# Kernel tuning notes

Measured on AMD Instinct MI355X. Metric: run time of the kernel, lower is better.

Reference implementation:

```python
import jax, jax.numpy as jnp
import numpy as np

J0 = -0.1
J1 = 0.1
ALPHA = 0.15
BUMP_WIDTH_FACTOR = 10.0


def _w_delta7(n):
    idx = jnp.arange(n, dtype=jnp.float32)
    angle_diff = 2.0 * jnp.pi * (idx[:, None] - idx[None, :]) / n
    return jnp.cos(angle_diff)  # [N, N]


def _initial_bump(batch_size, n):
    # initial angle = pi for every batch element (matches r_init=None path)
    angles = jnp.full((batch_size,), jnp.pi, dtype=jnp.float32)
    centers = (angles * n / (2.0 * jnp.pi))[:, None]          # [B, 1]
    width = n / BUMP_WIDTH_FACTOR
    idx = jnp.arange(n, dtype=jnp.float32)[None, :]            # [1, N]
    d = jnp.abs(idx - centers)
    dist = jnp.minimum(d, n - d)                               # circular distance
    bump = jnp.exp(-(dist ** 2) / (2.0 * width ** 2))
    return bump / jnp.linalg.norm(bump, axis=1, keepdims=True)  # [B, N]


def setup_inputs() -> dict:
    key = jax.random.key(0)
    k1, k2, k3 = jax.random.split(key, 3)
    B, S, A, N = 64, 256, 32, 256
    action_signal = jax.random.normal(k1, (B, S, A), dtype=jnp.float32)
    Wo = jax.random.normal(k2, (N, N), dtype=jnp.float32) / np.sqrt(N)
    Wa = jax.random.normal(k3, (A, N, N), dtype=jnp.float32) / np.sqrt(N)
    return {"action_signal": action_signal, "Wo": Wo, "Wa": Wa}


def reference(action_signal, Wo, Wa):
    B, S, A = action_signal.shape
    N = Wo.shape[0]
    W_delta7 = _w_delta7(N)
    r0 = _initial_bump(B, N)
    # static part of the effective weight matrix: J1*W_delta7 + Wo
    W_static = J1 * W_delta7 + Wo  # [N, N]

    def step(r, a_t):
        # a_t: [B, A], r: [B, N]
        # W_eff = J0 + W_static + sum_a a_t[a]*Wa[a]; rec = W_eff @ r (per batch)
        Wa_weighted = jnp.einsum('ba,anm->bnm', a_t, Wa)       # [B, N, N]
        rec = (J0 * jnp.sum(r, axis=-1, keepdims=True)
               + r @ W_static.T
               + jnp.einsum('bnm,bm->bn', Wa_weighted, r))      # [B, N]
        r_new = (1.0 - ALPHA) * r + ALPHA * jax.nn.relu(rec)
        return r_new, r_new

    _, bumps = jax.lax.scan(step, r0, jnp.swapaxes(action_signal, 0, 1))
    bump_history = jnp.swapaxes(bumps, 0, 1)                   # [B, S, N]
    r_delta7 = bump_history @ W_delta7                          # [B, S, N]
    r_history = r_delta7 / jnp.max(r_delta7, axis=2, keepdims=True)
    return r_history, bump_history
```

## Files before the change

kernel.cpp:

```cpp
#include <hip/hip_runtime.h>
#include <math.h>

#define N_    256
#define B_    64
#define S_    256
#define A_    32
#define NSZ   8
#define BSZ   8
#define LROWS 18
#define ATS   12
#define AROWS 33
#define J0_   (-0.1f)
#define J1_   (0.1f)
#define ALPHA_ 0.15f
#define WIDTH_ 25.6f
#define TWO_PI 6.283185307179586f

#define RPAR      (BSZ * N_)
#define RGRP      (2 * RPAR)
#define FLAG_OFF  (8 * RGRP)

#define WA_LDS_FLOATS (NSZ * LROWS * N_)
#define AT_LDS_FLOATS (2 * AROWS * ATS)
#define RLDS_FLOATS   (RPAR)
#define LDS_BYTES ((WA_LDS_FLOATS + AT_LDS_FLOATS + RLDS_FLOATS) * 4)

#define NN ((size_t)N_ * N_)

typedef float v2f __attribute__((ext_vector_type(2)));

#define LOADX4_COH(dst, p) \
  asm volatile("global_load_dwordx4 %0, %1, off sc0 sc1" \
               : "=v"(dst) : "v"(p) : "memory")
#define LOADX4(dst, p) \
  asm volatile("global_load_dwordx4 %0, %1, off" : "=v"(dst) : "v"(p) : "memory")
#define WAIT_VM0() asm volatile("s_waitcnt vmcnt(0)" ::: "memory")

#define ROWFMA(wvec, a_idx) do {                                              \
    const float* atp_ = atb + (a_idx) * ATS;                                  \
    const float4 t0_ = *reinterpret_cast<const float4*>(atp_);                \
    const float4 t1_ = *reinterpret_cast<const float4*>(atp_ + 4);            \
    const v2f at0_ = {t0_.x, t0_.y}, at1_ = {t0_.z, t0_.w};                   \
    const v2f at2_ = {t1_.x, t1_.y}, at3_ = {t1_.z, t1_.w};                   \
    const v2f wx_ = {(wvec).x, (wvec).x}, wy_ = {(wvec).y, (wvec).y};         \
    const v2f wz_ = {(wvec).z, (wvec).z}, ww_ = {(wvec).w, (wvec).w};         \
    const v2f d0_ = wx_*rrp[0][0] + wy_*rrp[0][1] + wz_*rrp[0][2] + ww_*rrp[0][3]; \
    const v2f d1_ = wx_*rrp[1][0] + wy_*rrp[1][1] + wz_*rrp[1][2] + ww_*rrp[1][3]; \
    const v2f d2_ = wx_*rrp[2][0] + wy_*rrp[2][1] + wz_*rrp[2][2] + ww_*rrp[2][3]; \
    const v2f d3_ = wx_*rrp[3][0] + wy_*rrp[3][1] + wz_*rrp[3][2] + ww_*rrp[3][3]; \
    accp[0] += at0_ * d0_;  accp[1] += at1_ * d1_;                            \
    accp[2] += at2_ * d2_;  accp[3] += at3_ * d3_;                            \
  } while (0)

__device__ __forceinline__ float bumpval(float idx) {
  float d = fabsf(idx - 128.0f);
  d = fminf(d, 256.0f - d);
  return expf(-d * d / (2.0f * WIDTH_ * WIDTH_));
}

__global__ __launch_bounds__(512, 1)
void ring_scan_kernel(const float* __restrict__ action,
                      const float* __restrict__ Wo,
                      const float* __restrict__ Wa,
                      float* __restrict__ out,
                      float* __restrict__ rws)
{
  extern __shared__ float lds[];
  float* wa_lds = lds;
  float* at_lds = lds + WA_LDS_FLOATS;
  float* r_lds  = lds + WA_LDS_FLOATS + AT_LDS_FLOATS;

  const int tid  = threadIdx.x;
  const int bid  = blockIdx.x;
  const int grp  = bid & 7;
  const int rank = bid >> 3;
  const int b0   = grp * BSZ;
  const int n0   = rank * NSZ;
  float*    rbase = rws + grp * RGRP;
  unsigned* flags = reinterpret_cast<unsigned*>(rws + FLAG_OFF) + grp * 32;

  for (int c = tid; c < NSZ * LROWS * (N_ / 4); c += 512) {
    const int rl = c >> 6;
    const int q  = c & 63;
    const int nl = rl / LROWS;
    const int a  = rl - nl * LROWS;
    const int n  = n0 + nl;
    float4 v;
    if (a < 17) {
      v = *reinterpret_cast<const float4*>(Wa + ((size_t)a * N_ + n) * N_ + q * 4);
    } else {
      const float4 wo = *reinterpret_cast<const float4*>(Wo + (size_t)n * N_ + q * 4);
      const float* wof = reinterpret_cast<const float*>(&wo);
      float tmp[4];
#pragma unroll
      for (int j = 0; j < 4; ++j) {
        const int m = q * 4 + j;
        tmp[j] = J0_ + J1_ * cosf((float)(n - m) * (TWO_PI / N_)) + wof[j];
      }
      v = make_float4(tmp[0], tmp[1], tmp[2], tmp[3]);
    }
    *reinterpret_cast<float4*>(wa_lds + rl * N_ + q * 4) = v;
  }
  if (tid < 16)
    at_lds[(tid >> 3) * (AROWS * ATS) + A_ * ATS + (tid & 7)] = 1.0f;
  if (tid < 256) {
    const int b = tid >> 5, a = tid & 31;
    at_lds[a * ATS + b] = action[((size_t)(b0 + b) * S_) * A_ + a];
  }

  const int wv = tid >> 6;
  const int mq = tid & 63;
  const int nG = n0 + wv;
  const float* wrow = wa_lds + wv * (LROWS * N_);
  const size_t bump_base = (size_t)B_ * S_ * N_;

  float4 sw0,sw1,sw2,sw3,sw4,sw5,sw6,sw7,sw8,sw9,sw10,sw11,sw12,sw13,sw14;
  {
    const float* wg = Wa + ((size_t)17 * N_ + nG) * N_ + mq * 4;
    LOADX4(sw0,  wg);           LOADX4(sw1,  wg + 1*NN);
    LOADX4(sw2,  wg + 2*NN);    LOADX4(sw3,  wg + 3*NN);
    LOADX4(sw4,  wg + 4*NN);    LOADX4(sw5,  wg + 5*NN);
    LOADX4(sw6,  wg + 6*NN);    LOADX4(sw7,  wg + 7*NN);
    LOADX4(sw8,  wg + 8*NN);    LOADX4(sw9,  wg + 9*NN);
    LOADX4(sw10, wg + 10*NN);   LOADX4(sw11, wg + 11*NN);
    LOADX4(sw12, wg + 12*NN);   LOADX4(sw13, wg + 13*NN);
    LOADX4(sw14, wg + 14*NN);
  }

  float g[4]; float ss = 0.0f;
#pragma unroll
  for (int j = 0; j < 4; ++j) { g[j] = bumpval((float)(mq * 4 + j)); ss += g[j] * g[j]; }
#pragma unroll
  for (int off = 1; off < 64; off <<= 1) ss += __shfl_xor(ss, off, 64);
  const float inv_norm = 1.0f / sqrtf(ss);

  v2f rrp[4][4];
#pragma unroll
  for (int p = 0; p < 4; ++p)
#pragma unroll
    for (int j = 0; j < 4; ++j) {
      const float rv = g[j] * inv_norm;
      rrp[p][j] = (v2f){rv, rv};
    }
  float rprev = (mq < 8) ? bumpval((float)nG) * inv_norm : 0.0f;

  __syncthreads();
  WAIT_VM0();

  for (int t = 0; t < S_; ++t) {
    const float* atb = at_lds + (t & 1) * (AROWS * ATS);

    if (t > 0) {
      const float* rsrc = rbase + ((t - 1) & 1) * RPAR;
      float4 rq;
      LOADX4_COH(rq, rsrc + tid * 4);
      WAIT_VM0();
      __builtin_amdgcn_sched_barrier(0);
      *reinterpret_cast<float4*>(r_lds + tid * 4) = rq;
      __syncthreads();
#pragma unroll
      for (int p = 0; p < 4; ++p) {
        const float4 ra = *reinterpret_cast<const float4*>(r_lds + (2*p)   * N_ + mq * 4);
        const float4 rb = *reinterpret_cast<const float4*>(r_lds + (2*p+1) * N_ + mq * 4);
        rrp[p][0] = (v2f){ra.x, rb.x};
        rrp[p][1] = (v2f){ra.y, rb.y};
        rrp[p][2] = (v2f){ra.z, rb.z};
        rrp[p][3] = (v2f){ra.w, rb.w};
      }
    }

    v2f accp[4];
#pragma unroll
    for (int p = 0; p < 4; ++p) accp[p] = (v2f){0.0f, 0.0f};

#pragma unroll
    for (int a = 0; a < LROWS; ++a) {
      const float4 w = *reinterpret_cast<const float4*>(wrow + a * N_ + mq * 4);
      ROWFMA(w, (a < 17) ? a : 32);
    }
    ROWFMA(sw0, 17);  ROWFMA(sw1, 18);  ROWFMA(sw2, 19);  ROWFMA(sw3, 20);
    ROWFMA(sw4, 21);  ROWFMA(sw5, 22);  ROWFMA(sw6, 23);  ROWFMA(sw7, 24);
    ROWFMA(sw8, 25);  ROWFMA(sw9, 26);  ROWFMA(sw10, 27); ROWFMA(sw11, 28);
    ROWFMA(sw12, 29); ROWFMA(sw13, 30); ROWFMA(sw14, 31);

    float acc[8];
#pragma unroll
    for (int p = 0; p < 4; ++p) { acc[2*p] = accp[p].x; acc[2*p+1] = accp[p].y; }

    const int bit0 = mq & 1, bit1 = mq & 2, bit2 = mq & 4;
    float t0 = bit0 ? acc[1] : acc[0], s0 = bit0 ? acc[0] : acc[1];
    float t1 = bit0 ? acc[3] : acc[2], s1 = bit0 ? acc[2] : acc[3];
    float t2 = bit0 ? acc[5] : acc[4], s2 = bit0 ? acc[4] : acc[5];
    float t3 = bit0 ? acc[7] : acc[6], s3 = bit0 ? acc[6] : acc[7];
    const float u0 = t0 + __shfl_xor(s0, 1, 64);
    const float u1 = t1 + __shfl_xor(s1, 1, 64);
    const float u2 = t2 + __shfl_xor(s2, 1, 64);
    const float u3 = t3 + __shfl_xor(s3, 1, 64);
    const float p0 = bit1 ? u1 : u0, q0 = bit1 ? u0 : u1;
    const float p1 = bit1 ? u3 : u2, q1 = bit1 ? u2 : u3;
    const float m0 = p0 + __shfl_xor(q0, 2, 64);
    const float m1 = p1 + __shfl_xor(q1, 2, 64);
    const float f0 = bit2 ? m1 : m0, g0 = bit2 ? m0 : m1;
    float f = f0 + __shfl_xor(g0, 4, 64);
    f += __shfl_xor(f, 8, 64);
    f += __shfl_xor(f, 16, 64);
    f += __shfl_xor(f, 32, 64);

    float rnew = 0.0f;
    if (mq < 8) {
      rnew = (1.0f - ALPHA_) * rprev + ALPHA_ * fmaxf(f, 0.0f);
      rprev = rnew;
      __hip_atomic_store(rbase + (t & 1) * RPAR + mq * N_ + nG, rnew,
                         __ATOMIC_RELAXED, __HIP_MEMORY_SCOPE_AGENT);
    }

    if (t == S_ - 1) {
      if (mq < 8)
        out[bump_base + ((size_t)(b0 + mq) * S_ + t) * N_ + nG] = rnew;
      break;
    }

    WAIT_VM0();
    __syncthreads();
    if (tid == 0)
      __hip_atomic_store(&flags[rank], (unsigned)(t + 1),
                         __ATOMIC_RELAXED, __HIP_MEMORY_SCOPE_AGENT);

    if (mq < 8)
      out[bump_base + ((size_t)(b0 + mq) * S_ + t) * N_ + nG] = rnew;
    if (tid < 256) {
      const int b = tid >> 5, a = tid & 31;
      at_lds[((t + 1) & 1) * (AROWS * ATS) + a * ATS + b] =
          action[((size_t)(b0 + b) * S_ + (t + 1)) * A_ + a];
    }

    if (wv == 0) {
      const unsigned tgt = (unsigned)(t + 1);
      while (true) {
        const unsigned fl = __hip_atomic_load(&flags[mq & 31], __ATOMIC_RELAXED,
                                              __HIP_MEMORY_SCOPE_AGENT);
        if (__all((int)(fl >= tgt))) break;
        __builtin_amdgcn_s_sleep(1);
      }
    }
    __syncthreads();
  }

  __threadfence();
  __syncthreads();
  if (tid == 0)
    __hip_atomic_store(&flags[rank], 256u, __ATOMIC_RELAXED,
                       __HIP_MEMORY_SCOPE_AGENT);
  if (wv == 0) {
    while (true) {
      const unsigned fl = __hip_atomic_load(&flags[mq & 31], __ATOMIC_RELAXED,
                                            __HIP_MEMORY_SCOPE_AGENT);
      if (__all((int)(fl >= 256u))) break;
      __builtin_amdgcn_s_sleep(1);
    }
  }
  __syncthreads();
  __threadfence();

  float cm[4], sm[4];
#pragma unroll
  for (int j = 0; j < 4; ++j) {
    const float ang = (float)(mq * 4 + j) * (TWO_PI / N_);
    cm[j] = cosf(ang);
    sm[j] = sinf(ang);
  }
  const float* bump = out + bump_base;
  for (int it = 0; it < 8; ++it) {
    const int row_local = rank * 64 + it * 8 + wv;
    const int b = b0 + (row_local >> 8);
    const int s = row_local & 255;
    const size_t row = (size_t)b * S_ + s;
    const float4 v = *reinterpret_cast<const float4*>(bump + row * N_ + mq * 4);
    float C  = cm[0]*v.x + cm[1]*v.y + cm[2]*v.z + cm[3]*v.w;
    float Sv = sm[0]*v.x + sm[1]*v.y + sm[2]*v.z + sm[3]*v.w;
#pragma unroll
    for (int off = 1; off < 64; off <<= 1) {
      C  += __shfl_xor(C,  off, 64);
      Sv += __shfl_xor(Sv, off, 64);
    }
    float y[4];
#pragma unroll
    for (int j = 0; j < 4; ++j) y[j] = cm[j] * C + sm[j] * Sv;
    float mx = fmaxf(fmaxf(y[0], y[1]), fmaxf(y[2], y[3]));
#pragma unroll
    for (int off = 1; off < 64; off <<= 1) mx = fmaxf(mx, __shfl_xor(mx, off, 64));
    const float inv = 1.0f / mx;
    *reinterpret_cast<float4*>(out + row * N_ + mq * 4) =
        make_float4(y[0] * inv, y[1] * inv, y[2] * inv, y[3] * inv);
  }
}

extern "C" void kernel_launch(void* const* d_in, const int* in_sizes, int n_in,
                              void* d_out, int out_size, void* d_ws, size_t ws_size,
                              hipStream_t stream) {
  const float* action = (const float*)d_in[0];
  const float* Wo     = (const float*)d_in[1];
  const float* Wa     = (const float*)d_in[2];
  float* out = (float*)d_out;
  float* rws = (float*)d_ws;

  (void)hipMemsetAsync((char*)d_ws + FLAG_OFF * sizeof(float), 0, 1024, stream);

  (void)hipFuncSetAttribute(reinterpret_cast<const void*>(ring_scan_kernel),
                            hipFuncAttributeMaxDynamicSharedMemorySize, LDS_BYTES);

  void* args[] = {(void*)&action, (void*)&Wo, (void*)&Wa, (void*)&out, (void*)&rws};
  (void)hipLaunchCooperativeKernel(reinterpret_cast<const void*>(ring_scan_kernel),
                                   dim3(256), dim3(512), args,
                                   (unsigned int)LDS_BYTES, stream);
}
```

Baseline: 1.433 ms.

## Move most Wa rows from LDS into registers and allow two blocks per CU

Shrinks the per-block LDS weight cache from 18 rows to 3 (two Wa rows plus the static row) and keeps the other 30 Wa rows resident in registers for the whole scan. The launch bound is raised to allow two 512-thread blocks per CU. The aim is to cut LDS footprint and LDS read traffic in the inner step and let the cross-block ring scan co-schedule. The cost is much higher register pressure: 120 extra floats per thread held alongside a lower register cap for two blocks per CU, which risks spills.

```diff
diff --git a/kernel.cpp b/kernel.cpp
--- a/kernel.cpp
+++ b/kernel.cpp
@@ -7,7 +7,7 @@
 #define A_    32
 #define NSZ   8
 #define BSZ   8
-#define LROWS 18
+#define LROWS 3
 #define ATS   12
 #define AROWS 33
 #define J0_   (-0.1f)
@@ -58,7 +58,7 @@
   return expf(-d * d / (2.0f * WIDTH_ * WIDTH_));
 }
 
-__global__ __launch_bounds__(512, 1)
+__global__ __launch_bounds__(512, 2)
 void ring_scan_kernel(const float* __restrict__ action,
                       const float* __restrict__ Wo,
                       const float* __restrict__ Wa,
@@ -86,7 +86,7 @@
     const int a  = rl - nl * LROWS;
     const int n  = n0 + nl;
     float4 v;
-    if (a < 17) {
+    if (a < 2) {
       v = *reinterpret_cast<const float4*>(Wa + ((size_t)a * N_ + n) * N_ + q * 4);
     } else {
       const float4 wo = *reinterpret_cast<const float4*>(Wo + (size_t)n * N_ + q * 4);
@@ -114,9 +114,11 @@
   const float* wrow = wa_lds + wv * (LROWS * N_);
   const size_t bump_base = (size_t)B_ * S_ * N_;
 
-  float4 sw0,sw1,sw2,sw3,sw4,sw5,sw6,sw7,sw8,sw9,sw10,sw11,sw12,sw13,sw14;
+  float4 sw0,sw1,sw2,sw3,sw4,sw5,sw6,sw7,sw8,sw9,sw10,sw11,sw12,sw13,sw14,
+         sw15,sw16,sw17,sw18,sw19,sw20,sw21,sw22,sw23,sw24,sw25,sw26,sw27,
+         sw28,sw29;
   {
-    const float* wg = Wa + ((size_t)17 * N_ + nG) * N_ + mq * 4;
+    const float* wg = Wa + ((size_t)2 * N_ + nG) * N_ + mq * 4;
     LOADX4(sw0,  wg);           LOADX4(sw1,  wg + 1*NN);
     LOADX4(sw2,  wg + 2*NN);    LOADX4(sw3,  wg + 3*NN);
     LOADX4(sw4,  wg + 4*NN);    LOADX4(sw5,  wg + 5*NN);
@@ -124,7 +126,14 @@
     LOADX4(sw8,  wg + 8*NN);    LOADX4(sw9,  wg + 9*NN);
     LOADX4(sw10, wg + 10*NN);   LOADX4(sw11, wg + 11*NN);
     LOADX4(sw12, wg + 12*NN);   LOADX4(sw13, wg + 13*NN);
-    LOADX4(sw14, wg + 14*NN);
+    LOADX4(sw14, wg + 14*NN);   LOADX4(sw15, wg + 15*NN);
+    LOADX4(sw16, wg + 16*NN);   LOADX4(sw17, wg + 17*NN);
+    LOADX4(sw18, wg + 18*NN);   LOADX4(sw19, wg + 19*NN);
+    LOADX4(sw20, wg + 20*NN);   LOADX4(sw21, wg + 21*NN);
+    LOADX4(sw22, wg + 22*NN);   LOADX4(sw23, wg + 23*NN);
+    LOADX4(sw24, wg + 24*NN);   LOADX4(sw25, wg + 25*NN);
+    LOADX4(sw26, wg + 26*NN);   LOADX4(sw27, wg + 27*NN);
+    LOADX4(sw28, wg + 28*NN);   LOADX4(sw29, wg + 29*NN);
   }
 
   float g[4]; float ss = 0.0f;
@@ -173,15 +182,22 @@
 #pragma unroll
     for (int p = 0; p < 4; ++p) accp[p] = (v2f){0.0f, 0.0f};
 
-#pragma unroll
-    for (int a = 0; a < LROWS; ++a) {
-      const float4 w = *reinterpret_cast<const float4*>(wrow + a * N_ + mq * 4);
-      ROWFMA(w, (a < 17) ? a : 32);
-    }
-    ROWFMA(sw0, 17);  ROWFMA(sw1, 18);  ROWFMA(sw2, 19);  ROWFMA(sw3, 20);
-    ROWFMA(sw4, 21);  ROWFMA(sw5, 22);  ROWFMA(sw6, 23);  ROWFMA(sw7, 24);
-    ROWFMA(sw8, 25);  ROWFMA(sw9, 26);  ROWFMA(sw10, 27); ROWFMA(sw11, 28);
-    ROWFMA(sw12, 29); ROWFMA(sw13, 30); ROWFMA(sw14, 31);
+    {
+      const float4 w0 = *reinterpret_cast<const float4*>(wrow + 0 * N_ + mq * 4);
+      ROWFMA(w0, 0);
+      const float4 w1 = *reinterpret_cast<const float4*>(wrow + 1 * N_ + mq * 4);
+      ROWFMA(w1, 1);
+      const float4 w2 = *reinterpret_cast<const float4*>(wrow + 2 * N_ + mq * 4);
+      ROWFMA(w2, 32);
+    }
+    ROWFMA(sw0,  2);  ROWFMA(sw1,  3);  ROWFMA(sw2,  4);  ROWFMA(sw3,  5);
+    ROWFMA(sw4,  6);  ROWFMA(sw5,  7);  ROWFMA(sw6,  8);  ROWFMA(sw7,  9);
+    ROWFMA(sw8,  10); ROWFMA(sw9,  11); ROWFMA(sw10, 12); ROWFMA(sw11, 13);
+    ROWFMA(sw12, 14); ROWFMA(sw13, 15); ROWFMA(sw14, 16); ROWFMA(sw15, 17);
+    ROWFMA(sw16, 18); ROWFMA(sw17, 19); ROWFMA(sw18, 20); ROWFMA(sw19, 21);
+    ROWFMA(sw20, 22); ROWFMA(sw21, 23); ROWFMA(sw22, 24); ROWFMA(sw23, 25);
+    ROWFMA(sw24, 26); ROWFMA(sw25, 27); ROWFMA(sw26, 28); ROWFMA(sw27, 29);
+    ROWFMA(sw28, 30); ROWFMA(sw29, 31);
 
     float acc[8];
 #pragma unroll
```

New measurement: 3.947 ms. 2.75x slower.
